# Kernel optimization log

Measured on AMD Instinct MI355X. Metric: run time of the kernel, lower is better.

## Reference

```python
import jax, jax.numpy as jnp
import numpy as np

D = 512
H = 8
DK = D // H
FF = 4 * D
EPS = 1e-5
NEG = -1.0e9


def _layernorm(x, g, b):
    mu = jnp.mean(x, axis=-1, keepdims=True)
    var = jnp.mean((x - mu) ** 2, axis=-1, keepdims=True)
    return (x - mu) * jax.lax.rsqrt(var + EPS) * g + b


def setup_inputs() -> dict:
    key = jax.random.key(0)
    ks = jax.random.split(key, 16)
    B, S = 4, 2048
    x = jax.random.normal(ks[0], (B, S, D), dtype=jnp.float32)
    # causal mask, broadcastable to [B, H, S, S]; mask==0 -> blocked
    mask = jnp.tril(jnp.ones((S, S), dtype=jnp.int32))[None, None]
    s = 1.0 / np.sqrt(D)
    sf = 1.0 / np.sqrt(FF)
    p = {
        "wq": jax.random.normal(ks[1], (D, D), jnp.float32) * s,
        "bq": jnp.zeros((D,), jnp.float32),
        "wk": jax.random.normal(ks[2], (D, D), jnp.float32) * s,
        "bk": jnp.zeros((D,), jnp.float32),
        "wv": jax.random.normal(ks[3], (D, D), jnp.float32) * s,
        "bv": jnp.zeros((D,), jnp.float32),
        "wo": jax.random.normal(ks[4], (D, D), jnp.float32) * s,
        "bo": jnp.zeros((D,), jnp.float32),
        "w1": jax.random.normal(ks[5], (D, FF), jnp.float32) * s,
        "b1": jnp.zeros((FF,), jnp.float32),
        "w2": jax.random.normal(ks[6], (FF, D), jnp.float32) * sf,
        "b2": jnp.zeros((D,), jnp.float32),
        "g1": jnp.ones((D,), jnp.float32),
        "be1": jnp.zeros((D,), jnp.float32),
        "g2": jnp.ones((D,), jnp.float32),
        "be2": jnp.zeros((D,), jnp.float32),
    }
    return {"x": x, "mask": mask, **p}


def reference(x, mask, wq, bq, wk, bk, wv, bv, wo, bo, w1, b1, w2, b2, g1, be1, g2, be2):
    B, S, _ = x.shape
    # projections -> [B, H, S, DK]
    q = (x @ wq + bq).reshape(B, S, H, DK).transpose(0, 2, 1, 3)
    k = (x @ wk + bk).reshape(B, S, H, DK).transpose(0, 2, 1, 3)
    v = (x @ wv + bv).reshape(B, S, H, DK).transpose(0, 2, 1, 3)
    scores = jnp.einsum("bhqd,bhkd->bhqk", q, k) / np.sqrt(DK)
    scores = jnp.where(mask == 0, NEG, scores)
    attn = jax.nn.softmax(scores, axis=-1)
    ctx = jnp.einsum("bhqk,bhkd->bhqd", attn, v)
    ctx = ctx.transpose(0, 2, 1, 3).reshape(B, S, D)
    attn_out = ctx @ wo + bo
    # dropout is inference-mode identity
    h = _layernorm(x + attn_out, g1, be1)
    ffn = jax.nn.relu(h @ w1 + b1) @ w2 + b2
    return _layernorm(h + ffn, g2, be2)
```

## Files before the change

kernel.cpp:

```cpp
#include <hip/hip_runtime.h>
#include <math.h>

#define D_   512
#define H_   8
#define DK_  64
#define FF_  2048
#define S_   2048
#define B_   4
#define M_   (B_*S_)
#define EPS_ 1e-5f
#define SCLQ 0.1803368801111f

typedef __attribute__((ext_vector_type(8))) short bf16x8;
typedef __attribute__((ext_vector_type(4))) float f32x4;
typedef __attribute__((ext_vector_type(4))) unsigned int u32x4;

__device__ inline unsigned short f2b(float f) {
    unsigned u = __builtin_bit_cast(unsigned, f);
    unsigned r = (u + 0x7FFFu + ((u >> 16) & 1u)) >> 16;
    return (unsigned short)r;
}
__device__ inline float b2f(unsigned short u) {
    return __builtin_bit_cast(float, (unsigned)u << 16);
}
__device__ inline unsigned packbf(float p0, float p1) {
    return (__builtin_bit_cast(unsigned, p1) & 0xFFFF0000u) |
           (__builtin_bit_cast(unsigned, p0) >> 16);
}

__device__ __forceinline__ void async_cp16(const void* g, void* l) {
    __builtin_amdgcn_global_load_lds(
        (const __attribute__((address_space(1))) unsigned int*)g,
        (__attribute__((address_space(3))) unsigned int*)l, 16, 0, 0);
}

__global__ __launch_bounds__(256)
void prep_kernel(const float* __restrict__ x,
                 const float* __restrict__ wq, const float* __restrict__ wk,
                 const float* __restrict__ wv, const float* __restrict__ wo,
                 const float* __restrict__ bq, const float* __restrict__ bk,
                 const float* __restrict__ bv,
                 const float* __restrict__ w1, const float* __restrict__ w2,
                 unsigned short* __restrict__ xb, unsigned short* __restrict__ wqkvt,
                 unsigned short* __restrict__ wot, unsigned short* __restrict__ w1t,
                 unsigned short* __restrict__ w2t, float* __restrict__ bqkv)
{
    __shared__ float L[32][33];
    const int bid = blockIdx.x;
    const int tid = threadIdx.x;

    if (bid < 2048) {
        const int i = (bid * 256 + tid) * 8;
        const float4 a = *(const float4*)(x + i);
        const float4 b = *(const float4*)(x + i + 4);
        bf16x8 v;
        v[0] = (short)f2b(a.x); v[1] = (short)f2b(a.y);
        v[2] = (short)f2b(a.z); v[3] = (short)f2b(a.w);
        v[4] = (short)f2b(b.x); v[5] = (short)f2b(b.y);
        v[6] = (short)f2b(b.z); v[7] = (short)f2b(b.w);
        *(bf16x8*)(xb + i) = v;
        return;
    }

    const float* w; unsigned short* wt; int K, N, k0, n0; float scl = 1.f;
    if (bid < 3072) {
        const int z = (bid - 2048) >> 8;
        const int r = (bid - 2048) & 255;
        n0 = (r & 15) * 32; k0 = (r >> 4) * 32; K = 512; N = 512;
        w  = (z == 0) ? wq : (z == 1) ? wk : (z == 2) ? wv : wo;
        wt = (z < 3) ? (wqkvt + (size_t)z * 512 * 512) : wot;
        if (z == 0) scl = SCLQ;
        if (z < 3 && r == 0) {
            const float* bsrc = (z == 0) ? bq : (z == 1) ? bk : bv;
            const float bscl  = (z == 0) ? SCLQ : 1.f;
            bqkv[z * 512 + tid]       = bsrc[tid] * bscl;
            bqkv[z * 512 + 256 + tid] = bsrc[256 + tid] * bscl;
        }
    } else if (bid < 4096) {
        const int r = bid - 3072;
        n0 = (r & 63) * 32; k0 = (r >> 6) * 32; K = 512; N = 2048;
        w = w1; wt = w1t;
    } else {
        const int r = bid - 4096;
        n0 = (r & 15) * 32; k0 = (r >> 4) * 32; K = 2048; N = 512;
        w = w2; wt = w2t;
    }

    const int xx = tid & 31, y = tid >> 5;
#pragma unroll
    for (int i = 0; i < 4; i++)
        L[y + i * 8][xx] = w[(size_t)(k0 + y + i * 8) * N + n0 + xx] * scl;
    __syncthreads();
#pragma unroll
    for (int i = 0; i < 4; i++)
        wt[(size_t)(n0 + y + i * 8) * K + k0 + xx] = f2b(L[xx][y + i * 8]);
}

template<int WR, int WC, int MT, int NT, int OUTB, int RELU, int RESADD, int HASBIAS>
__global__ __launch_bounds__(256)
void gemm_bf16(const unsigned short* __restrict__ A, const unsigned short* __restrict__ Bt,
               const float* __restrict__ bias, const void* __restrict__ RES,
               void* __restrict__ Cv, int K, int lda, int ldb, int ldc)
{
    constexpr int BM = WR * MT * 16;
    constexpr int BN = WC * NT * 16;
    constexpr int CA = BM / 64;
    constexpr int CB = BN / 64;
    __shared__ unsigned short As[2][BM * 32];
    __shared__ unsigned short Bs[2][BN * 32];

    const int tid  = threadIdx.x;
    const int lane = tid & 63;
    const int w    = tid >> 6;
    const int wr   = w / WC, wc = w % WC;
    const int quad = lane >> 4;
    const int l15  = lane & 15;
    const int n0   = blockIdx.x * BN;
    const int m0   = blockIdx.y * BM;

    f32x4 acc[MT][NT];
#pragma unroll
    for (int i = 0; i < MT; i++)
#pragma unroll
        for (int j = 0; j < NT; j++) acc[i][j] = (f32x4){0.f, 0.f, 0.f, 0.f};

    auto stage = [&](int k0, int bufi) {
#pragma unroll
        for (int i = 0; i < CA; i++) {
            const int c = tid + i * 256;
            async_cp16(&A[(size_t)(m0 + (c >> 2)) * lda + k0 + (c & 3) * 8], &As[bufi][c * 8]);
        }
#pragma unroll
        for (int i = 0; i < CB; i++) {
            const int c = tid + i * 256;
            async_cp16(&Bt[(size_t)(n0 + (c >> 2)) * ldb + k0 + (c & 3) * 8], &Bs[bufi][c * 8]);
        }
    };

    stage(0, 0);
    const int niter = K >> 5;
    for (int ii = 0; ii < niter; ii++) {
        const int knext = (ii + 1 < niter) ? (ii + 1) * 32 : 0;
        stage(knext, (ii + 1) & 1);
        __builtin_amdgcn_s_waitcnt(0x0f70 | (CA + CB));
        __builtin_amdgcn_s_barrier();

        const unsigned short* Ac = &As[ii & 1][0];
        const unsigned short* Bc = &Bs[ii & 1][0];
        bf16x8 af[MT], bfr[NT];
#pragma unroll
        for (int t = 0; t < MT; t++)
            af[t]  = *(const bf16x8*)&Ac[(wr * MT * 16 + t * 16 + l15) * 32 + quad * 8];
#pragma unroll
        for (int t = 0; t < NT; t++)
            bfr[t] = *(const bf16x8*)&Bc[(wc * NT * 16 + t * 16 + l15) * 32 + quad * 8];
#pragma unroll
        for (int mt = 0; mt < MT; mt++)
#pragma unroll
            for (int nt = 0; nt < NT; nt++)
                acc[mt][nt] = __builtin_amdgcn_mfma_f32_16x16x32_bf16(
                    af[mt], bfr[nt], acc[mt][nt], 0, 0, 0);
        __builtin_amdgcn_s_barrier();
    }

#pragma unroll
    for (int mt = 0; mt < MT; mt++) {
        const int rowb = m0 + wr * MT * 16 + mt * 16 + quad * 4;
#pragma unroll
        for (int nt = 0; nt < NT; nt++) {
            const int col = n0 + wc * NT * 16 + nt * 16 + l15;
            const float bv = HASBIAS ? bias[col] : 0.f;
#pragma unroll
            for (int r = 0; r < 4; r++) {
                const size_t idx = (size_t)(rowb + r) * ldc + col;
                float v = acc[mt][nt][r] + bv;
                if (RESADD == 1) v += ((const float*)RES)[idx];
                if (RESADD == 2) v += b2f(((const unsigned short*)RES)[idx]);
                if (RELU)   v = fmaxf(v, 0.f);
                if (OUTB) ((unsigned short*)Cv)[idx] = f2b(v);
                else      ((float*)Cv)[idx] = v;
            }
        }
    }
}

__global__ __launch_bounds__(256)
void vtrans(const unsigned short* __restrict__ qkv, unsigned short* __restrict__ vt)
{
    __shared__ unsigned short L[64][72];
    const int s0 = blockIdx.x * 64;
    const int bh = blockIdx.y;
    const int b  = bh >> 3, hh = bh & 7;
    const int tid = threadIdx.x;
    const unsigned short* src = qkv + (size_t)(b * S_) * 1536 + 1024 + hh * 64;
#pragma unroll
    for (int i = 0; i < 2; i++) {
        const int c = tid + i * 256;
        const int r = c >> 3, sub = (c & 7) * 8;
        *(bf16x8*)&L[r][sub] = *(const bf16x8*)(src + (size_t)(s0 + r) * 1536 + sub);
    }
    __syncthreads();
    const int dk = tid >> 2;
    const int sc = (tid & 3) * 16;
    bf16x8 t0, t1;
#pragma unroll
    for (int j = 0; j < 8; j++) t0[j] = (short)L[sc + j][dk];
#pragma unroll
    for (int j = 0; j < 8; j++) t1[j] = (short)L[sc + 8 + j][dk];
    unsigned short* dst = vt + (size_t)(bh * 64 + dk) * S_ + s0 + sc;
    *(bf16x8*)(dst)     = t0;
    *(bf16x8*)(dst + 8) = t1;
}

__global__ __launch_bounds__(256, 4)
void attn_mfma(const unsigned short* __restrict__ qkv,
               const unsigned short* __restrict__ vt,
               unsigned short* __restrict__ ctx)
{
    __shared__ unsigned short Ks[2][64 * 64];
    __shared__ unsigned short Vs[2][64 * 64];

    const int tid  = threadIdx.x;
    const int lane = tid & 63;
    const int w    = tid >> 6;
    const int quad = lane >> 4;
    const int l15  = lane & 15;
    const int bid  = blockIdx.x;
    const int qb   = 31 - (bid >> 5);
    const int bh   = bid & 31;
    const int b    = bh >> 3, hh = bh & 7;

    const unsigned short* qbase = qkv + (size_t)(b * S_) * 1536 + hh * 64;
    const unsigned short* kbase = qbase + 512;
    const unsigned short* vtb   = vt + (size_t)bh * 64 * S_;

    const int srcA  = 32 * (quad & 1) + l15;
    const int srcB  = srcA + 16;
    const bool selHi = (quad >> 1) != 0;

    bf16x8 ones;
#pragma unroll
    for (int j = 0; j < 8; j++) ones[j] = (short)0x3F80;

    auto stage = [&](int kb, int bufi) {
        unsigned short* kd = &Ks[bufi][0];
        unsigned short* vd = &Vs[bufi][0];
#pragma unroll
        for (int i = 0; i < 2; i++) {
            const int c = tid + i * 256;
            const int row = c >> 3;
            const int l = (c & 7) ^ (row & 7);
            async_cp16(kbase + (size_t)(kb * 64 + row) * 1536 + l * 8, kd + c * 8);
            async_cp16(vtb + (size_t)row * S_ + kb * 64 + l * 8, vd + c * 8);
        }
    };

    const int qrow0 = qb * 64 + w * 16;
    bf16x8 qf[2];
    {
        const unsigned short* qr = qbase + (size_t)(qrow0 + l15) * 1536;
        qf[0] = *(const bf16x8*)(qr + quad * 8);
        qf[1] = *(const bf16x8*)(qr + 32 + quad * 8);
    }

    f32x4 Oacc[5];
#pragma unroll
    for (int i = 0; i < 5; i++) Oacc[i] = (f32x4){0.f, 0.f, 0.f, 0.f};

    stage(0, 0);

    auto pv_chunk = [&](const unsigned pk[4][2], int kc, const unsigned short* Vc) {
        const unsigned tA0 = __shfl(pk[kc * 2][0],     srcA, 64);
        const unsigned tA1 = __shfl(pk[kc * 2][1],     srcA, 64);
        const unsigned tB0 = __shfl(pk[kc * 2 + 1][0], srcA, 64);
        const unsigned tB1 = __shfl(pk[kc * 2 + 1][1], srcA, 64);
        const unsigned uA0 = __shfl(pk[kc * 2][0],     srcB, 64);
        const unsigned uA1 = __shfl(pk[kc * 2][1],     srcB, 64);
        const unsigned uB0 = __shfl(pk[kc * 2 + 1][0], srcB, 64);
        const unsigned uB1 = __shfl(pk[kc * 2 + 1][1], srcB, 64);
        u32x4 a;
        a[0] = selHi ? tB0 : tA0;
        a[1] = selHi ? tB1 : tA1;
        a[2] = selHi ? uB0 : uA0;
        a[3] = selHi ? uB1 : uA1;
        const bf16x8 af = __builtin_bit_cast(bf16x8, a);
#pragma unroll
        for (int nt = 0; nt < 4; nt++) {
            const int phys = (kc * 4 + quad) ^ (l15 & 7);
            const bf16x8 vf = *(const bf16x8*)&Vc[(nt * 16 + l15) * 64 + phys * 8];
            Oacc[nt] = __builtin_amdgcn_mfma_f32_16x16x32_bf16(af, vf, Oacc[nt], 0, 0, 0);
        }
        Oacc[4] = __builtin_amdgcn_mfma_f32_16x16x32_bf16(af, ones, Oacc[4], 0, 0, 0);
    };

    for (int kb = 0; kb < qb; kb++) {
        stage(kb + 1, (kb + 1) & 1);
        __builtin_amdgcn_s_waitcnt(0x0F74);
        __builtin_amdgcn_s_barrier();
        const unsigned short* Kc = &Ks[kb & 1][0];
        const unsigned short* Vc = &Vs[kb & 1][0];

        f32x4 st[4];
#pragma unroll
        for (int nt = 0; nt < 4; nt++) st[nt] = (f32x4){0.f, 0.f, 0.f, 0.f};
#pragma unroll
        for (int kc = 0; kc < 2; kc++)
#pragma unroll
            for (int nt = 0; nt < 4; nt++) {
                const int phys = (kc * 4 + quad) ^ (l15 & 7);
                const bf16x8 kf = *(const bf16x8*)&Kc[(nt * 16 + l15) * 64 + phys * 8];
                st[nt] = __builtin_amdgcn_mfma_f32_16x16x32_bf16(kf, qf[kc], st[nt], 0, 0, 0);
            }

        unsigned pk[4][2];
#pragma unroll
        for (int nt = 0; nt < 4; nt++) {
            const float p0 = exp2f(st[nt][0]);
            const float p1 = exp2f(st[nt][1]);
            const float p2 = exp2f(st[nt][2]);
            const float p3 = exp2f(st[nt][3]);
            pk[nt][0] = packbf(p0, p1);
            pk[nt][1] = packbf(p2, p3);
        }

        pv_chunk(pk, 0, Vc);
        pv_chunk(pk, 1, Vc);
        __builtin_amdgcn_s_barrier();
    }

    {
        stage(0, (qb + 1) & 1);
        __builtin_amdgcn_s_waitcnt(0x0F74);
        __builtin_amdgcn_s_barrier();
        const unsigned short* Kc = &Ks[qb & 1][0];
        const unsigned short* Vc = &Vs[qb & 1][0];

        f32x4 st[4];
#pragma unroll
        for (int nt = 0; nt < 4; nt++) st[nt] = (f32x4){0.f, 0.f, 0.f, 0.f};
#pragma unroll
        for (int kc = 0; kc < 2; kc++)
#pragma unroll
            for (int nt = 0; nt < 4; nt++) {
                if (nt > w) continue;
                const int phys = (kc * 4 + quad) ^ (l15 & 7);
                const bf16x8 kf = *(const bf16x8*)&Kc[(nt * 16 + l15) * 64 + phys * 8];
                st[nt] = __builtin_amdgcn_mfma_f32_16x16x32_bf16(kf, qf[kc], st[nt], 0, 0, 0);
            }

        const int rhs = w * 16 + l15;
        unsigned pk[4][2];
#pragma unroll
        for (int nt = 0; nt < 4; nt++) {
            const int kb0 = nt * 16 + quad * 4;
            float p[4];
#pragma unroll
            for (int r = 0; r < 4; r++) {
                float s = st[nt][r];
                if (kb0 + r > rhs) s = -1.0e9f;
                p[r] = exp2f(s);
            }
            pk[nt][0] = packbf(p[0], p[1]);
            pk[nt][1] = packbf(p[2], p[3]);
        }

        const int kc_d = (w >> 1) + 1;
        pv_chunk(pk, 0, Vc);
        if (kc_d > 1) pv_chunk(pk, 1, Vc);
    }

    const int orow = qrow0 + quad * 4;
    unsigned short* cb = ctx + (size_t)(b * S_) * 512 + hh * 64;
#pragma unroll
    for (int r = 0; r < 4; r++) {
        const float inv = 1.f / Oacc[4][r];
#pragma unroll
        for (int nt = 0; nt < 4; nt++)
            cb[(size_t)(orow + r) * 512 + nt * 16 + l15] = f2b(Oacc[nt][r] * inv);
    }
}

template<int WF, int WB>
__global__ __launch_bounds__(256)
void ln_kernel(const float* __restrict__ s, const float* __restrict__ g,
               const float* __restrict__ be, float* __restrict__ out,
               unsigned short* __restrict__ outb)
{
    const int wave = threadIdx.x >> 6;
    const int lane = threadIdx.x & 63;
    const int row  = blockIdx.x * 4 + wave;
    const float* ps = s + (size_t)row * D_;
    const int c0 = lane * 4;

    float v[8];
    {
        const float4 a0 = *(const float4*)(ps + c0);
        const float4 a1 = *(const float4*)(ps + c0 + 256);
        v[0] = a0.x; v[1] = a0.y; v[2] = a0.z; v[3] = a0.w;
        v[4] = a1.x; v[5] = a1.y; v[6] = a1.z; v[7] = a1.w;
    }

    float sum = 0.f;
#pragma unroll
    for (int i = 0; i < 8; i++) sum += v[i];
#pragma unroll
    for (int m = 1; m < 64; m <<= 1) sum += __shfl_xor(sum, m);
    const float mu = sum * (1.f / D_);

    float sq = 0.f;
#pragma unroll
    for (int i = 0; i < 8; i++) { const float d = v[i] - mu; sq += d * d; }
#pragma unroll
    for (int m = 1; m < 64; m <<= 1) sq += __shfl_xor(sq, m);
    const float rstd = rsqrtf(sq * (1.f / D_) + EPS_);

    const float4 g0 = *(const float4*)(g + c0);
    const float4 b0 = *(const float4*)(be + c0);
    const float4 g1 = *(const float4*)(g + c0 + 256);
    const float4 b1 = *(const float4*)(be + c0 + 256);

    float o[8];
    o[0] = (v[0] - mu) * rstd * g0.x + b0.x;
    o[1] = (v[1] - mu) * rstd * g0.y + b0.y;
    o[2] = (v[2] - mu) * rstd * g0.z + b0.z;
    o[3] = (v[3] - mu) * rstd * g0.w + b0.w;
    o[4] = (v[4] - mu) * rstd * g1.x + b1.x;
    o[5] = (v[5] - mu) * rstd * g1.y + b1.y;
    o[6] = (v[6] - mu) * rstd * g1.z + b1.z;
    o[7] = (v[7] - mu) * rstd * g1.w + b1.w;

    if (WF) {
        *(float4*)(out + (size_t)row * D_ + c0)       = *(float4*)&o[0];
        *(float4*)(out + (size_t)row * D_ + c0 + 256) = *(float4*)&o[4];
    }
    if (WB) {
        short4 vb0 = (short4){(short)f2b(o[0]), (short)f2b(o[1]), (short)f2b(o[2]), (short)f2b(o[3])};
        short4 vb1 = (short4){(short)f2b(o[4]), (short)f2b(o[5]), (short)f2b(o[6]), (short)f2b(o[7])};
        *(short4*)(outb + (size_t)row * D_ + c0)       = vb0;
        *(short4*)(outb + (size_t)row * D_ + c0 + 256) = vb1;
    }
}

extern "C" void kernel_launch(void* const* d_in, const int* in_sizes, int n_in,
                              void* d_out, int out_size, void* d_ws, size_t ws_size,
                              hipStream_t stream)
{
    const float* x  = (const float*)d_in[0];
    const float* wq = (const float*)d_in[2];
    const float* bq = (const float*)d_in[3];
    const float* wk = (const float*)d_in[4];
    const float* bk = (const float*)d_in[5];
    const float* wv = (const float*)d_in[6];
    const float* bv = (const float*)d_in[7];
    const float* wo = (const float*)d_in[8];
    const float* bo = (const float*)d_in[9];
    const float* w1 = (const float*)d_in[10];
    const float* b1 = (const float*)d_in[11];
    const float* w2 = (const float*)d_in[12];
    const float* b2 = (const float*)d_in[13];
    const float* g1 = (const float*)d_in[14];
    const float* be1= (const float*)d_in[15];
    const float* g2 = (const float*)d_in[16];
    const float* be2= (const float*)d_in[17];
    float* out = (float*)d_out;

    const size_t MB = 1048576;
    char* w8 = (char*)d_ws;
    unsigned short* wqkvt = (unsigned short*)(w8 + 0);
    unsigned short* wot   = (unsigned short*)(w8 + 1572864);
    unsigned short* w1t   = (unsigned short*)(w8 + 2097152);
    unsigned short* w2t   = (unsigned short*)(w8 + 4194304);
    float*          bqkv  = (float*)(w8 + 6291456);
    unsigned short* qkv   = (unsigned short*)(w8 + 8 * MB);
    unsigned short* ffn1b = qkv;
    unsigned short* xb    = (unsigned short*)(w8 + 40 * MB);
    unsigned short* ctx   = xb;
    unsigned short* vt    = (unsigned short*)(w8 + 48 * MB);
    unsigned short* hb    = vt;
    float*          pre   = (float*)(w8 + 56 * MB);

    const dim3 blk(256);

    prep_kernel<<<dim3(5120), blk, 0, stream>>>(
        x, wq, wk, wv, wo, bq, bk, bv, w1, w2, xb, wqkvt, wot, w1t, w2t, bqkv);

    gemm_bf16<2,2,4,4,1,0,0,1><<<dim3(12, 64), blk, 0, stream>>>(
        xb, wqkvt, bqkv, nullptr, qkv, 512, 512, 512, 1536);

    vtrans<<<dim3(32, 32), blk, 0, stream>>>(qkv, vt);

    attn_mfma<<<dim3(1024), blk, 0, stream>>>(qkv, vt, ctx);

    gemm_bf16<2,2,2,4,0,0,1,1><<<dim3(4, 128), blk, 0, stream>>>(
        ctx, wot, bo, x, pre, 512, 512, 512, 512);

    ln_kernel<0,1><<<dim3(M_ / 4), blk, 0, stream>>>(pre, g1, be1, nullptr, hb);

    gemm_bf16<2,2,4,4,1,1,0,1><<<dim3(16, 64), blk, 0, stream>>>(
        hb, w1t, b1, nullptr, ffn1b, 512, 512, 512, 2048);

    gemm_bf16<2,2,2,4,0,0,2,1><<<dim3(4, 128), blk, 0, stream>>>(
        ffn1b, w2t, b2, hb, pre, 2048, 2048, 2048, 512);

    ln_kernel<1,0><<<dim3(M_ / 4), blk, 0, stream>>>(pre, g2, be2, out, nullptr);
}
```

Baseline: 289.7 us.

## Process two 64-row query tiles per attention block to reuse staged K/V

Each attention workgroup now covers 128 query rows as two 64-row sub-tiles that share every staged K/V tile from LDS, so the grid is halved to 512 blocks. The causal diagonal is handled by two special iterations with per-sub-tile masking. The query-block order is changed to interleave long and short blocks so the causal work is spread more evenly. Register use goes up (doubled accumulators and Q fragments) and the launch-bounds occupancy hint drops from 4 to 2, which may lower latency hiding.

```diff
diff --git a/kernel.cpp b/kernel.cpp
--- a/kernel.cpp
+++ b/kernel.cpp
@@ -212,7 +212,7 @@
     *(bf16x8*)(dst + 8) = t1;
 }
 
-__global__ __launch_bounds__(256, 4)
+__global__ __launch_bounds__(256, 2)
 void attn_mfma(const unsigned short* __restrict__ qkv,
                const unsigned short* __restrict__ vt,
                unsigned short* __restrict__ ctx)
@@ -225,9 +225,9 @@
     const int w    = tid >> 6;
     const int quad = lane >> 4;
     const int l15  = lane & 15;
-    const int bid  = blockIdx.x;
-    const int qb   = 31 - (bid >> 5);
-    const int bh   = bid & 31;
+    const int g    = blockIdx.x >> 5;
+    const int qb   = (g < 8) ? (15 - g) : (g - 8);
+    const int bh   = blockIdx.x & 31;
     const int b    = bh >> 3, hh = bh & 7;
 
     const unsigned short* qbase = qkv + (size_t)(b * S_) * 1536 + hh * 64;
@@ -255,21 +255,23 @@
         }
     };
 
-    const int qrow0 = qb * 64 + w * 16;
-    bf16x8 qf[2];
-    {
-        const unsigned short* qr = qbase + (size_t)(qrow0 + l15) * 1536;
-        qf[0] = *(const bf16x8*)(qr + quad * 8);
-        qf[1] = *(const bf16x8*)(qr + 32 + quad * 8);
-    }
-
-    f32x4 Oacc[5];
-#pragma unroll
-    for (int i = 0; i < 5; i++) Oacc[i] = (f32x4){0.f, 0.f, 0.f, 0.f};
+    bf16x8 qf[2][2];
+#pragma unroll
+    for (int mt = 0; mt < 2; mt++) {
+        const unsigned short* qr = qbase + (size_t)(qb * 128 + mt * 64 + w * 16 + l15) * 1536;
+        qf[mt][0] = *(const bf16x8*)(qr + quad * 8);
+        qf[mt][1] = *(const bf16x8*)(qr + 32 + quad * 8);
+    }
+
+    f32x4 Oacc[2][5];
+#pragma unroll
+    for (int mt = 0; mt < 2; mt++)
+#pragma unroll
+        for (int i = 0; i < 5; i++) Oacc[mt][i] = (f32x4){0.f, 0.f, 0.f, 0.f};
 
     stage(0, 0);
 
-    auto pv_chunk = [&](const unsigned pk[4][2], int kc, const unsigned short* Vc) {
+    auto assemble = [&](const unsigned pk[4][2], int kc) -> bf16x8 {
         const unsigned tA0 = __shfl(pk[kc * 2][0],     srcA, 64);
         const unsigned tA1 = __shfl(pk[kc * 2][1],     srcA, 64);
         const unsigned tB0 = __shfl(pk[kc * 2 + 1][0], srcA, 64);
@@ -283,57 +285,132 @@
         a[1] = selHi ? tB1 : tA1;
         a[2] = selHi ? uB0 : uA0;
         a[3] = selHi ? uB1 : uA1;
-        const bf16x8 af = __builtin_bit_cast(bf16x8, a);
-#pragma unroll
-        for (int nt = 0; nt < 4; nt++) {
-            const int phys = (kc * 4 + quad) ^ (l15 & 7);
-            const bf16x8 vf = *(const bf16x8*)&Vc[(nt * 16 + l15) * 64 + phys * 8];
-            Oacc[nt] = __builtin_amdgcn_mfma_f32_16x16x32_bf16(af, vf, Oacc[nt], 0, 0, 0);
-        }
-        Oacc[4] = __builtin_amdgcn_mfma_f32_16x16x32_bf16(af, ones, Oacc[4], 0, 0, 0);
+        return __builtin_bit_cast(bf16x8, a);
     };
 
-    for (int kb = 0; kb < qb; kb++) {
+    const int nmain = 2 * qb;
+
+    for (int kb = 0; kb < nmain; kb++) {
         stage(kb + 1, (kb + 1) & 1);
         __builtin_amdgcn_s_waitcnt(0x0F74);
         __builtin_amdgcn_s_barrier();
         const unsigned short* Kc = &Ks[kb & 1][0];
         const unsigned short* Vc = &Vs[kb & 1][0];
 
-        f32x4 st[4];
-#pragma unroll
-        for (int nt = 0; nt < 4; nt++) st[nt] = (f32x4){0.f, 0.f, 0.f, 0.f};
+        f32x4 st[2][4];
+#pragma unroll
+        for (int mt = 0; mt < 2; mt++)
+#pragma unroll
+            for (int nt = 0; nt < 4; nt++) st[mt][nt] = (f32x4){0.f, 0.f, 0.f, 0.f};
 #pragma unroll
         for (int kc = 0; kc < 2; kc++)
 #pragma unroll
             for (int nt = 0; nt < 4; nt++) {
                 const int phys = (kc * 4 + quad) ^ (l15 & 7);
                 const bf16x8 kf = *(const bf16x8*)&Kc[(nt * 16 + l15) * 64 + phys * 8];
-                st[nt] = __builtin_amdgcn_mfma_f32_16x16x32_bf16(kf, qf[kc], st[nt], 0, 0, 0);
-            }
-
-        unsigned pk[4][2];
+                st[0][nt] = __builtin_amdgcn_mfma_f32_16x16x32_bf16(kf, qf[0][kc], st[0][nt], 0, 0, 0);
+                st[1][nt] = __builtin_amdgcn_mfma_f32_16x16x32_bf16(kf, qf[1][kc], st[1][nt], 0, 0, 0);
+            }
+
+        unsigned pk[2][4][2];
+#pragma unroll
+        for (int mt = 0; mt < 2; mt++)
+#pragma unroll
+            for (int nt = 0; nt < 4; nt++) {
+                pk[mt][nt][0] = packbf(exp2f(st[mt][nt][0]), exp2f(st[mt][nt][1]));
+                pk[mt][nt][1] = packbf(exp2f(st[mt][nt][2]), exp2f(st[mt][nt][3]));
+            }
+
+#pragma unroll
+        for (int kc = 0; kc < 2; kc++) {
+            const bf16x8 af0 = assemble(pk[0], kc);
+            const bf16x8 af1 = assemble(pk[1], kc);
+#pragma unroll
+            for (int nt = 0; nt < 4; nt++) {
+                const int phys = (kc * 4 + quad) ^ (l15 & 7);
+                const bf16x8 vf = *(const bf16x8*)&Vc[(nt * 16 + l15) * 64 + phys * 8];
+                Oacc[0][nt] = __builtin_amdgcn_mfma_f32_16x16x32_bf16(af0, vf, Oacc[0][nt], 0, 0, 0);
+                Oacc[1][nt] = __builtin_amdgcn_mfma_f32_16x16x32_bf16(af1, vf, Oacc[1][nt], 0, 0, 0);
+            }
+            Oacc[0][4] = __builtin_amdgcn_mfma_f32_16x16x32_bf16(af0, ones, Oacc[0][4], 0, 0, 0);
+            Oacc[1][4] = __builtin_amdgcn_mfma_f32_16x16x32_bf16(af1, ones, Oacc[1][4], 0, 0, 0);
+        }
+        __builtin_amdgcn_s_barrier();
+    }
+
+    const int rhs  = w * 16 + l15;
+    const int kc_d = (w >> 1) + 1;
+
+    {
+        stage(nmain + 1, (nmain + 1) & 1);
+        __builtin_amdgcn_s_waitcnt(0x0F74);
+        __builtin_amdgcn_s_barrier();
+        const unsigned short* Kc = &Ks[nmain & 1][0];
+        const unsigned short* Vc = &Vs[nmain & 1][0];
+
+        f32x4 st[2][4];
+#pragma unroll
+        for (int mt = 0; mt < 2; mt++)
+#pragma unroll
+            for (int nt = 0; nt < 4; nt++) st[mt][nt] = (f32x4){0.f, 0.f, 0.f, 0.f};
+#pragma unroll
+        for (int kc = 0; kc < 2; kc++)
+#pragma unroll
+            for (int nt = 0; nt < 4; nt++) {
+                const int phys = (kc * 4 + quad) ^ (l15 & 7);
+                const bf16x8 kf = *(const bf16x8*)&Kc[(nt * 16 + l15) * 64 + phys * 8];
+                if (nt <= w)
+                    st[0][nt] = __builtin_amdgcn_mfma_f32_16x16x32_bf16(kf, qf[0][kc], st[0][nt], 0, 0, 0);
+                st[1][nt] = __builtin_amdgcn_mfma_f32_16x16x32_bf16(kf, qf[1][kc], st[1][nt], 0, 0, 0);
+            }
+
+        unsigned pk[2][4][2];
 #pragma unroll
         for (int nt = 0; nt < 4; nt++) {
-            const float p0 = exp2f(st[nt][0]);
-            const float p1 = exp2f(st[nt][1]);
-            const float p2 = exp2f(st[nt][2]);
-            const float p3 = exp2f(st[nt][3]);
-            pk[nt][0] = packbf(p0, p1);
-            pk[nt][1] = packbf(p2, p3);
-        }
-
-        pv_chunk(pk, 0, Vc);
-        pv_chunk(pk, 1, Vc);
+            const int kb0 = nt * 16 + quad * 4;
+            float p[4];
+#pragma unroll
+            for (int r = 0; r < 4; r++) {
+                float s = st[0][nt][r];
+                if (kb0 + r > rhs) s = -1.0e9f;
+                p[r] = exp2f(s);
+            }
+            pk[0][nt][0] = packbf(p[0], p[1]);
+            pk[0][nt][1] = packbf(p[2], p[3]);
+            pk[1][nt][0] = packbf(exp2f(st[1][nt][0]), exp2f(st[1][nt][1]));
+            pk[1][nt][1] = packbf(exp2f(st[1][nt][2]), exp2f(st[1][nt][3]));
+        }
+
+#pragma unroll
+        for (int kc = 0; kc < 2; kc++) {
+            const bf16x8 af1 = assemble(pk[1], kc);
+#pragma unroll
+            for (int nt = 0; nt < 4; nt++) {
+                const int phys = (kc * 4 + quad) ^ (l15 & 7);
+                const bf16x8 vf = *(const bf16x8*)&Vc[(nt * 16 + l15) * 64 + phys * 8];
+                Oacc[1][nt] = __builtin_amdgcn_mfma_f32_16x16x32_bf16(af1, vf, Oacc[1][nt], 0, 0, 0);
+            }
+            Oacc[1][4] = __builtin_amdgcn_mfma_f32_16x16x32_bf16(af1, ones, Oacc[1][4], 0, 0, 0);
+            if (kc < kc_d) {
+                const bf16x8 af0 = assemble(pk[0], kc);
+#pragma unroll
+                for (int nt = 0; nt < 4; nt++) {
+                    const int phys = (kc * 4 + quad) ^ (l15 & 7);
+                    const bf16x8 vf = *(const bf16x8*)&Vc[(nt * 16 + l15) * 64 + phys * 8];
+                    Oacc[0][nt] = __builtin_amdgcn_mfma_f32_16x16x32_bf16(af0, vf, Oacc[0][nt], 0, 0, 0);
+                }
+                Oacc[0][4] = __builtin_amdgcn_mfma_f32_16x16x32_bf16(af0, ones, Oacc[0][4], 0, 0, 0);
+            }
+        }
         __builtin_amdgcn_s_barrier();
     }
 
     {
-        stage(0, (qb + 1) & 1);
+        stage(0, nmain & 1);
         __builtin_amdgcn_s_waitcnt(0x0F74);
         __builtin_amdgcn_s_barrier();
-        const unsigned short* Kc = &Ks[qb & 1][0];
-        const unsigned short* Vc = &Vs[qb & 1][0];
+        const unsigned short* Kc = &Ks[(nmain + 1) & 1][0];
+        const unsigned short* Vc = &Vs[(nmain + 1) & 1][0];
 
         f32x4 st[4];
 #pragma unroll
@@ -345,10 +422,9 @@
                 if (nt > w) continue;
                 const int phys = (kc * 4 + quad) ^ (l15 & 7);
                 const bf16x8 kf = *(const bf16x8*)&Kc[(nt * 16 + l15) * 64 + phys * 8];
-                st[nt] = __builtin_amdgcn_mfma_f32_16x16x32_bf16(kf, qf[kc], st[nt], 0, 0, 0);
-            }
-
-        const int rhs = w * 16 + l15;
+                st[nt] = __builtin_amdgcn_mfma_f32_16x16x32_bf16(kf, qf[1][kc], st[nt], 0, 0, 0);
+            }
+
         unsigned pk[4][2];
 #pragma unroll
         for (int nt = 0; nt < 4; nt++) {
@@ -364,19 +440,32 @@
             pk[nt][1] = packbf(p[2], p[3]);
         }
 
-        const int kc_d = (w >> 1) + 1;
-        pv_chunk(pk, 0, Vc);
-        if (kc_d > 1) pv_chunk(pk, 1, Vc);
-    }
-
-    const int orow = qrow0 + quad * 4;
+#pragma unroll
+        for (int kc = 0; kc < 2; kc++) {
+            if (kc < kc_d) {
+                const bf16x8 af = assemble(pk, kc);
+#pragma unroll
+                for (int nt = 0; nt < 4; nt++) {
+                    const int phys = (kc * 4 + quad) ^ (l15 & 7);
+                    const bf16x8 vf = *(const bf16x8*)&Vc[(nt * 16 + l15) * 64 + phys * 8];
+                    Oacc[1][nt] = __builtin_amdgcn_mfma_f32_16x16x32_bf16(af, vf, Oacc[1][nt], 0, 0, 0);
+                }
+                Oacc[1][4] = __builtin_amdgcn_mfma_f32_16x16x32_bf16(af, ones, Oacc[1][4], 0, 0, 0);
+            }
+        }
+    }
+
     unsigned short* cb = ctx + (size_t)(b * S_) * 512 + hh * 64;
 #pragma unroll
-    for (int r = 0; r < 4; r++) {
-        const float inv = 1.f / Oacc[4][r];
-#pragma unroll
-        for (int nt = 0; nt < 4; nt++)
-            cb[(size_t)(orow + r) * 512 + nt * 16 + l15] = f2b(Oacc[nt][r] * inv);
+    for (int mt = 0; mt < 2; mt++) {
+        const int orow = qb * 128 + mt * 64 + w * 16 + quad * 4;
+#pragma unroll
+        for (int r = 0; r < 4; r++) {
+            const float inv = 1.f / Oacc[mt][4][r];
+#pragma unroll
+            for (int nt = 0; nt < 4; nt++)
+                cb[(size_t)(orow + r) * 512 + nt * 16 + l15] = f2b(Oacc[mt][nt][r] * inv);
+        }
     }
 }
 
@@ -489,7 +578,7 @@
 
     vtrans<<<dim3(32, 32), blk, 0, stream>>>(qkv, vt);
 
-    attn_mfma<<<dim3(1024), blk, 0, stream>>>(qkv, vt, ctx);
+    attn_mfma<<<dim3(512), blk, 0, stream>>>(qkv, vt, ctx);
 
     gemm_bf16<2,2,2,4,0,0,1,1><<<dim3(4, 128), blk, 0, stream>>>(
         ctx, wot, bo, x, pre, 512, 512, 512, 512);
```

Result: slower. 295.6 us (+2.0%).

## Fuse V transpose into QKV GEMM epilogue and drop vtrans kernel

Applied to the files above, without the earlier changes.

The QKV projection GEMM now writes the V portion directly in transposed per-head layout (dk-major, sequence contiguous) from its epilogue, and only Q and K go into a narrower row buffer with stride 1024. This removes the separate vtrans kernel launch and its extra read and write of V. Attention occupancy hint is also raised from 4 to 5 blocks per SM. The transposed stores are only 8-byte short4 writes with a 4 KB stride between lanes, so they may coalesce poorly, and the higher occupancy hint may cause register spills.

```diff
diff --git a/kernel.cpp b/kernel.cpp
--- a/kernel.cpp
+++ b/kernel.cpp
@@ -96,11 +96,12 @@
         wt[(size_t)(n0 + y + i * 8) * K + k0 + xx] = f2b(L[xx][y + i * 8]);
 }
 
-template<int WR, int WC, int MT, int NT, int OUTB, int RELU, int RESADD, int HASBIAS>
+template<int WR, int WC, int MT, int NT, int OUTB, int RELU, int RESADD, int HASBIAS, int QKVW>
 __global__ __launch_bounds__(256)
 void gemm_bf16(const unsigned short* __restrict__ A, const unsigned short* __restrict__ Bt,
                const float* __restrict__ bias, const void* __restrict__ RES,
-               void* __restrict__ Cv, int K, int lda, int ldb, int ldc)
+               void* __restrict__ Cv, unsigned short* __restrict__ vtout,
+               int K, int lda, int ldb, int ldc)
 {
     constexpr int BM = WR * MT * 16;
     constexpr int BN = WC * NT * 16;
@@ -163,6 +164,28 @@
         __builtin_amdgcn_s_barrier();
     }
 
+    if (QKVW && n0 >= 1024) {
+#pragma unroll
+        for (int mt = 0; mt < MT; mt++) {
+            const int rowb = m0 + wr * MT * 16 + mt * 16 + quad * 4;
+            const int bb   = rowb >> 11;
+            const int s0   = rowb & 2047;
+#pragma unroll
+            for (int nt = 0; nt < NT; nt++) {
+                const int col = n0 + wc * NT * 16 + nt * 16 + l15;
+                const int hh  = (col - 1024) >> 6;
+                const int dk  = (col - 1024) & 63;
+                const float bv = bias[col];
+                short4 pk4;
+                pk4.x = (short)f2b(acc[mt][nt][0] + bv);
+                pk4.y = (short)f2b(acc[mt][nt][1] + bv);
+                pk4.z = (short)f2b(acc[mt][nt][2] + bv);
+                pk4.w = (short)f2b(acc[mt][nt][3] + bv);
+                *(short4*)(vtout + ((size_t)((bb * 8 + hh) * 64 + dk)) * S_ + s0) = pk4;
+            }
+        }
+        return;
+    }
 #pragma unroll
     for (int mt = 0; mt < MT; mt++) {
         const int rowb = m0 + wr * MT * 16 + mt * 16 + quad * 4;
@@ -184,36 +207,8 @@
     }
 }
 
-__global__ __launch_bounds__(256)
-void vtrans(const unsigned short* __restrict__ qkv, unsigned short* __restrict__ vt)
-{
-    __shared__ unsigned short L[64][72];
-    const int s0 = blockIdx.x * 64;
-    const int bh = blockIdx.y;
-    const int b  = bh >> 3, hh = bh & 7;
-    const int tid = threadIdx.x;
-    const unsigned short* src = qkv + (size_t)(b * S_) * 1536 + 1024 + hh * 64;
-#pragma unroll
-    for (int i = 0; i < 2; i++) {
-        const int c = tid + i * 256;
-        const int r = c >> 3, sub = (c & 7) * 8;
-        *(bf16x8*)&L[r][sub] = *(const bf16x8*)(src + (size_t)(s0 + r) * 1536 + sub);
-    }
-    __syncthreads();
-    const int dk = tid >> 2;
-    const int sc = (tid & 3) * 16;
-    bf16x8 t0, t1;
-#pragma unroll
-    for (int j = 0; j < 8; j++) t0[j] = (short)L[sc + j][dk];
-#pragma unroll
-    for (int j = 0; j < 8; j++) t1[j] = (short)L[sc + 8 + j][dk];
-    unsigned short* dst = vt + (size_t)(bh * 64 + dk) * S_ + s0 + sc;
-    *(bf16x8*)(dst)     = t0;
-    *(bf16x8*)(dst + 8) = t1;
-}
-
-__global__ __launch_bounds__(256, 4)
-void attn_mfma(const unsigned short* __restrict__ qkv,
+__global__ __launch_bounds__(256, 5)
+void attn_mfma(const unsigned short* __restrict__ qk,
                const unsigned short* __restrict__ vt,
                unsigned short* __restrict__ ctx)
 {
@@ -230,7 +225,7 @@
     const int bh   = bid & 31;
     const int b    = bh >> 3, hh = bh & 7;
 
-    const unsigned short* qbase = qkv + (size_t)(b * S_) * 1536 + hh * 64;
+    const unsigned short* qbase = qk + (size_t)(b * S_) * 1024 + hh * 64;
     const unsigned short* kbase = qbase + 512;
     const unsigned short* vtb   = vt + (size_t)bh * 64 * S_;
 
@@ -250,7 +245,7 @@
             const int c = tid + i * 256;
             const int row = c >> 3;
             const int l = (c & 7) ^ (row & 7);
-            async_cp16(kbase + (size_t)(kb * 64 + row) * 1536 + l * 8, kd + c * 8);
+            async_cp16(kbase + (size_t)(kb * 64 + row) * 1024 + l * 8, kd + c * 8);
             async_cp16(vtb + (size_t)row * S_ + kb * 64 + l * 8, vd + c * 8);
         }
     };
@@ -258,7 +253,7 @@
     const int qrow0 = qb * 64 + w * 16;
     bf16x8 qf[2];
     {
-        const unsigned short* qr = qbase + (size_t)(qrow0 + l15) * 1536;
+        const unsigned short* qr = qbase + (size_t)(qrow0 + l15) * 1024;
         qf[0] = *(const bf16x8*)(qr + quad * 8);
         qf[1] = *(const bf16x8*)(qr + 32 + quad * 8);
     }
@@ -315,12 +310,8 @@
         unsigned pk[4][2];
 #pragma unroll
         for (int nt = 0; nt < 4; nt++) {
-            const float p0 = exp2f(st[nt][0]);
-            const float p1 = exp2f(st[nt][1]);
-            const float p2 = exp2f(st[nt][2]);
-            const float p3 = exp2f(st[nt][3]);
-            pk[nt][0] = packbf(p0, p1);
-            pk[nt][1] = packbf(p2, p3);
+            pk[nt][0] = packbf(exp2f(st[nt][0]), exp2f(st[nt][1]));
+            pk[nt][1] = packbf(exp2f(st[nt][2]), exp2f(st[nt][3]));
         }
 
         pv_chunk(pk, 0, Vc);
@@ -471,8 +462,8 @@
     unsigned short* w1t   = (unsigned short*)(w8 + 2097152);
     unsigned short* w2t   = (unsigned short*)(w8 + 4194304);
     float*          bqkv  = (float*)(w8 + 6291456);
-    unsigned short* qkv   = (unsigned short*)(w8 + 8 * MB);
-    unsigned short* ffn1b = qkv;
+    unsigned short* qk    = (unsigned short*)(w8 + 8 * MB);
+    unsigned short* ffn1b = qk;
     unsigned short* xb    = (unsigned short*)(w8 + 40 * MB);
     unsigned short* ctx   = xb;
     unsigned short* vt    = (unsigned short*)(w8 + 48 * MB);
@@ -484,23 +475,21 @@
     prep_kernel<<<dim3(5120), blk, 0, stream>>>(
         x, wq, wk, wv, wo, bq, bk, bv, w1, w2, xb, wqkvt, wot, w1t, w2t, bqkv);
 
-    gemm_bf16<2,2,4,4,1,0,0,1><<<dim3(12, 64), blk, 0, stream>>>(
-        xb, wqkvt, bqkv, nullptr, qkv, 512, 512, 512, 1536);
-
-    vtrans<<<dim3(32, 32), blk, 0, stream>>>(qkv, vt);
-
-    attn_mfma<<<dim3(1024), blk, 0, stream>>>(qkv, vt, ctx);
-
-    gemm_bf16<2,2,2,4,0,0,1,1><<<dim3(4, 128), blk, 0, stream>>>(
-        ctx, wot, bo, x, pre, 512, 512, 512, 512);
+    gemm_bf16<2,2,4,4,1,0,0,1,1><<<dim3(12, 64), blk, 0, stream>>>(
+        xb, wqkvt, bqkv, nullptr, qk, vt, 512, 512, 512, 1024);
+
+    attn_mfma<<<dim3(1024), blk, 0, stream>>>(qk, vt, ctx);
+
+    gemm_bf16<2,2,2,4,0,0,1,1,0><<<dim3(4, 128), blk, 0, stream>>>(
+        ctx, wot, bo, x, pre, nullptr, 512, 512, 512, 512);
 
     ln_kernel<0,1><<<dim3(M_ / 4), blk, 0, stream>>>(pre, g1, be1, nullptr, hb);
 
-    gemm_bf16<2,2,4,4,1,1,0,1><<<dim3(16, 64), blk, 0, stream>>>(
-        hb, w1t, b1, nullptr, ffn1b, 512, 512, 512, 2048);
-
-    gemm_bf16<2,2,2,4,0,0,2,1><<<dim3(4, 128), blk, 0, stream>>>(
-        ffn1b, w2t, b2, hb, pre, 2048, 2048, 2048, 512);
+    gemm_bf16<2,2,4,4,1,1,0,1,0><<<dim3(16, 64), blk, 0, stream>>>(
+        hb, w1t, b1, nullptr, ffn1b, nullptr, 512, 512, 512, 2048);
+
+    gemm_bf16<2,2,2,4,0,0,2,1,0><<<dim3(4, 128), blk, 0, stream>>>(
+        ffn1b, w2t, b2, hb, pre, nullptr, 2048, 2048, 2048, 512);
 
     ln_kernel<1,0><<<dim3(M_ / 4), blk, 0, stream>>>(pre, g2, be2, out, nullptr);
 }
```

New measurement: 293.4 us. Within noise of the previous version (+1.3%).

## Split attention waves over 2x2 query/key halves with LDS reduction of partial outputs

Applied to the files above, without the earlier changes.

Each wave now covers 32 query rows and one 32-key half of every key block instead of 16 query rows over all 64 keys. Every K and V fragment read from LDS therefore feeds two query tiles, and the diagonal block skips fully masked wave combinations. The two key-half partial accumulators are added through LDS at the end. This cuts LDS fragment traffic per MFMA, at the cost of more accumulator registers, extra barriers and a final reduction pass.

```diff
diff --git a/kernel.cpp b/kernel.cpp
--- a/kernel.cpp
+++ b/kernel.cpp
@@ -229,6 +229,8 @@
     const int qb   = 31 - (bid >> 5);
     const int bh   = bid & 31;
     const int b    = bh >> 3, hh = bh & 7;
+    const int kh   = w & 1;
+    const int qh   = w >> 1;
 
     const unsigned short* qbase = qkv + (size_t)(b * S_) * 1536 + hh * 64;
     const unsigned short* kbase = qbase + 512;
@@ -255,43 +257,40 @@
         }
     };
 
-    const int qrow0 = qb * 64 + w * 16;
-    bf16x8 qf[2];
-    {
-        const unsigned short* qr = qbase + (size_t)(qrow0 + l15) * 1536;
-        qf[0] = *(const bf16x8*)(qr + quad * 8);
-        qf[1] = *(const bf16x8*)(qr + 32 + quad * 8);
-    }
-
-    f32x4 Oacc[5];
-#pragma unroll
-    for (int i = 0; i < 5; i++) Oacc[i] = (f32x4){0.f, 0.f, 0.f, 0.f};
+    bf16x8 qf[2][2];
+#pragma unroll
+    for (int qt = 0; qt < 2; qt++) {
+        const unsigned short* qr = qbase + (size_t)(qb * 64 + qh * 32 + qt * 16 + l15) * 1536;
+        qf[qt][0] = *(const bf16x8*)(qr + quad * 8);
+        qf[qt][1] = *(const bf16x8*)(qr + 32 + quad * 8);
+    }
+
+    f32x4 Oacc[2][5];
+#pragma unroll
+    for (int qt = 0; qt < 2; qt++)
+#pragma unroll
+        for (int i = 0; i < 5; i++) Oacc[qt][i] = (f32x4){0.f, 0.f, 0.f, 0.f};
 
     stage(0, 0);
 
-    auto pv_chunk = [&](const unsigned pk[4][2], int kc, const unsigned short* Vc) {
-        const unsigned tA0 = __shfl(pk[kc * 2][0],     srcA, 64);
-        const unsigned tA1 = __shfl(pk[kc * 2][1],     srcA, 64);
-        const unsigned tB0 = __shfl(pk[kc * 2 + 1][0], srcA, 64);
-        const unsigned tB1 = __shfl(pk[kc * 2 + 1][1], srcA, 64);
-        const unsigned uA0 = __shfl(pk[kc * 2][0],     srcB, 64);
-        const unsigned uA1 = __shfl(pk[kc * 2][1],     srcB, 64);
-        const unsigned uB0 = __shfl(pk[kc * 2 + 1][0], srcB, 64);
-        const unsigned uB1 = __shfl(pk[kc * 2 + 1][1], srcB, 64);
+    auto assemble2 = [&](const unsigned t0[2], const unsigned t1[2]) -> bf16x8 {
+        const unsigned a0A = __shfl(t0[0], srcA, 64);
+        const unsigned a1A = __shfl(t0[1], srcA, 64);
+        const unsigned b0A = __shfl(t1[0], srcA, 64);
+        const unsigned b1A = __shfl(t1[1], srcA, 64);
+        const unsigned a0B = __shfl(t0[0], srcB, 64);
+        const unsigned a1B = __shfl(t0[1], srcB, 64);
+        const unsigned b0B = __shfl(t1[0], srcB, 64);
+        const unsigned b1B = __shfl(t1[1], srcB, 64);
         u32x4 a;
-        a[0] = selHi ? tB0 : tA0;
-        a[1] = selHi ? tB1 : tA1;
-        a[2] = selHi ? uB0 : uA0;
-        a[3] = selHi ? uB1 : uA1;
-        const bf16x8 af = __builtin_bit_cast(bf16x8, a);
-#pragma unroll
-        for (int nt = 0; nt < 4; nt++) {
-            const int phys = (kc * 4 + quad) ^ (l15 & 7);
-            const bf16x8 vf = *(const bf16x8*)&Vc[(nt * 16 + l15) * 64 + phys * 8];
-            Oacc[nt] = __builtin_amdgcn_mfma_f32_16x16x32_bf16(af, vf, Oacc[nt], 0, 0, 0);
-        }
-        Oacc[4] = __builtin_amdgcn_mfma_f32_16x16x32_bf16(af, ones, Oacc[4], 0, 0, 0);
+        a[0] = selHi ? b0A : a0A;
+        a[1] = selHi ? b1A : a1A;
+        a[2] = selHi ? b0B : a0B;
+        a[3] = selHi ? b1B : a1B;
+        return __builtin_bit_cast(bf16x8, a);
     };
+
+    const int physv = (kh * 4 + quad) ^ (l15 & 7);
 
     for (int kb = 0; kb < qb; kb++) {
         stage(kb + 1, (kb + 1) & 1);
@@ -300,31 +299,44 @@
         const unsigned short* Kc = &Ks[kb & 1][0];
         const unsigned short* Vc = &Vs[kb & 1][0];
 
-        f32x4 st[4];
-#pragma unroll
-        for (int nt = 0; nt < 4; nt++) st[nt] = (f32x4){0.f, 0.f, 0.f, 0.f};
-#pragma unroll
-        for (int kc = 0; kc < 2; kc++)
-#pragma unroll
-            for (int nt = 0; nt < 4; nt++) {
-                const int phys = (kc * 4 + quad) ^ (l15 & 7);
-                const bf16x8 kf = *(const bf16x8*)&Kc[(nt * 16 + l15) * 64 + phys * 8];
-                st[nt] = __builtin_amdgcn_mfma_f32_16x16x32_bf16(kf, qf[kc], st[nt], 0, 0, 0);
-            }
-
-        unsigned pk[4][2];
-#pragma unroll
-        for (int nt = 0; nt < 4; nt++) {
-            const float p0 = exp2f(st[nt][0]);
-            const float p1 = exp2f(st[nt][1]);
-            const float p2 = exp2f(st[nt][2]);
-            const float p3 = exp2f(st[nt][3]);
-            pk[nt][0] = packbf(p0, p1);
-            pk[nt][1] = packbf(p2, p3);
-        }
-
-        pv_chunk(pk, 0, Vc);
-        pv_chunk(pk, 1, Vc);
+        f32x4 st[2][2];
+#pragma unroll
+        for (int qt = 0; qt < 2; qt++)
+#pragma unroll
+            for (int kt = 0; kt < 2; kt++) st[qt][kt] = (f32x4){0.f, 0.f, 0.f, 0.f};
+#pragma unroll
+        for (int kc = 0; kc < 2; kc++) {
+            const int phys = (kc * 4 + quad) ^ (l15 & 7);
+            const bf16x8 kf0 = *(const bf16x8*)&Kc[(kh * 32 + l15) * 64 + phys * 8];
+            const bf16x8 kf1 = *(const bf16x8*)&Kc[(kh * 32 + 16 + l15) * 64 + phys * 8];
+#pragma unroll
+            for (int qt = 0; qt < 2; qt++) {
+                st[qt][0] = __builtin_amdgcn_mfma_f32_16x16x32_bf16(kf0, qf[qt][kc], st[qt][0], 0, 0, 0);
+                st[qt][1] = __builtin_amdgcn_mfma_f32_16x16x32_bf16(kf1, qf[qt][kc], st[qt][1], 0, 0, 0);
+            }
+        }
+
+        unsigned pk[2][2][2];
+#pragma unroll
+        for (int qt = 0; qt < 2; qt++)
+#pragma unroll
+            for (int kt = 0; kt < 2; kt++) {
+                pk[qt][kt][0] = packbf(exp2f(st[qt][kt][0]), exp2f(st[qt][kt][1]));
+                pk[qt][kt][1] = packbf(exp2f(st[qt][kt][2]), exp2f(st[qt][kt][3]));
+            }
+
+        bf16x8 vf[4];
+#pragma unroll
+        for (int nt = 0; nt < 4; nt++)
+            vf[nt] = *(const bf16x8*)&Vc[(nt * 16 + l15) * 64 + physv * 8];
+#pragma unroll
+        for (int qt = 0; qt < 2; qt++) {
+            const bf16x8 af = assemble2(pk[qt][0], pk[qt][1]);
+#pragma unroll
+            for (int nt = 0; nt < 4; nt++)
+                Oacc[qt][nt] = __builtin_amdgcn_mfma_f32_16x16x32_bf16(af, vf[nt], Oacc[qt][nt], 0, 0, 0);
+            Oacc[qt][4] = __builtin_amdgcn_mfma_f32_16x16x32_bf16(af, ones, Oacc[qt][4], 0, 0, 0);
+        }
         __builtin_amdgcn_s_barrier();
     }
 
@@ -335,48 +347,98 @@
         const unsigned short* Kc = &Ks[qb & 1][0];
         const unsigned short* Vc = &Vs[qb & 1][0];
 
-        f32x4 st[4];
-#pragma unroll
-        for (int nt = 0; nt < 4; nt++) st[nt] = (f32x4){0.f, 0.f, 0.f, 0.f};
-#pragma unroll
-        for (int kc = 0; kc < 2; kc++)
-#pragma unroll
-            for (int nt = 0; nt < 4; nt++) {
-                if (nt > w) continue;
+        const bool skipDiag = (kh == 1 && qh == 0);
+        const bool fullDiag = (kh == 0 && qh == 1);
+
+        if (!skipDiag) {
+            f32x4 st[2][2];
+#pragma unroll
+            for (int qt = 0; qt < 2; qt++)
+#pragma unroll
+                for (int kt = 0; kt < 2; kt++) st[qt][kt] = (f32x4){0.f, 0.f, 0.f, 0.f};
+#pragma unroll
+            for (int kc = 0; kc < 2; kc++) {
                 const int phys = (kc * 4 + quad) ^ (l15 & 7);
-                const bf16x8 kf = *(const bf16x8*)&Kc[(nt * 16 + l15) * 64 + phys * 8];
-                st[nt] = __builtin_amdgcn_mfma_f32_16x16x32_bf16(kf, qf[kc], st[nt], 0, 0, 0);
-            }
-
-        const int rhs = w * 16 + l15;
-        unsigned pk[4][2];
-#pragma unroll
-        for (int nt = 0; nt < 4; nt++) {
-            const int kb0 = nt * 16 + quad * 4;
-            float p[4];
+                const bf16x8 kf0 = *(const bf16x8*)&Kc[(kh * 32 + l15) * 64 + phys * 8];
+                const bf16x8 kf1 = *(const bf16x8*)&Kc[(kh * 32 + 16 + l15) * 64 + phys * 8];
+#pragma unroll
+                for (int qt = 0; qt < 2; qt++) {
+                    st[qt][0] = __builtin_amdgcn_mfma_f32_16x16x32_bf16(kf0, qf[qt][kc], st[qt][0], 0, 0, 0);
+                    st[qt][1] = __builtin_amdgcn_mfma_f32_16x16x32_bf16(kf1, qf[qt][kc], st[qt][1], 0, 0, 0);
+                }
+            }
+
+            unsigned pk[2][2][2];
+            if (fullDiag) {
+#pragma unroll
+                for (int qt = 0; qt < 2; qt++)
+#pragma unroll
+                    for (int kt = 0; kt < 2; kt++) {
+                        pk[qt][kt][0] = packbf(exp2f(st[qt][kt][0]), exp2f(st[qt][kt][1]));
+                        pk[qt][kt][1] = packbf(exp2f(st[qt][kt][2]), exp2f(st[qt][kt][3]));
+                    }
+            } else {
+                float p[4];
+#pragma unroll
+                for (int r = 0; r < 4; r++)
+                    p[r] = (quad * 4 + r > l15) ? 0.f : exp2f(st[0][0][r]);
+                pk[0][0][0] = packbf(p[0], p[1]);
+                pk[0][0][1] = packbf(p[2], p[3]);
+                pk[0][1][0] = 0u; pk[0][1][1] = 0u;
+                pk[1][0][0] = packbf(exp2f(st[1][0][0]), exp2f(st[1][0][1]));
+                pk[1][0][1] = packbf(exp2f(st[1][0][2]), exp2f(st[1][0][3]));
+#pragma unroll
+                for (int r = 0; r < 4; r++)
+                    p[r] = (quad * 4 + r > l15) ? 0.f : exp2f(st[1][1][r]);
+                pk[1][1][0] = packbf(p[0], p[1]);
+                pk[1][1][1] = packbf(p[2], p[3]);
+            }
+
+            bf16x8 vf[4];
+#pragma unroll
+            for (int nt = 0; nt < 4; nt++)
+                vf[nt] = *(const bf16x8*)&Vc[(nt * 16 + l15) * 64 + physv * 8];
+#pragma unroll
+            for (int qt = 0; qt < 2; qt++) {
+                const bf16x8 af = assemble2(pk[qt][0], pk[qt][1]);
+#pragma unroll
+                for (int nt = 0; nt < 4; nt++)
+                    Oacc[qt][nt] = __builtin_amdgcn_mfma_f32_16x16x32_bf16(af, vf[nt], Oacc[qt][nt], 0, 0, 0);
+                Oacc[qt][4] = __builtin_amdgcn_mfma_f32_16x16x32_bf16(af, ones, Oacc[qt][4], 0, 0, 0);
+            }
+        }
+    }
+
+    __syncthreads();
+    float* red = (float*)&Ks[0][0];
+    const int rbase = (qh * 64 + lane) * 44;
+    if (kh) {
+#pragma unroll
+        for (int qt = 0; qt < 2; qt++)
+#pragma unroll
+            for (int i = 0; i < 5; i++)
+                *(f32x4*)&red[rbase + (qt * 5 + i) * 4] = Oacc[qt][i];
+    }
+    __syncthreads();
+    if (!kh) {
+#pragma unroll
+        for (int qt = 0; qt < 2; qt++)
+#pragma unroll
+            for (int i = 0; i < 5; i++)
+                Oacc[qt][i] += *(const f32x4*)&red[rbase + (qt * 5 + i) * 4];
+
+        unsigned short* cb = ctx + (size_t)(b * S_) * 512 + hh * 64;
+#pragma unroll
+        for (int qt = 0; qt < 2; qt++) {
+            const int orow = qb * 64 + qh * 32 + qt * 16 + quad * 4;
 #pragma unroll
             for (int r = 0; r < 4; r++) {
-                float s = st[nt][r];
-                if (kb0 + r > rhs) s = -1.0e9f;
-                p[r] = exp2f(s);
-            }
-            pk[nt][0] = packbf(p[0], p[1]);
-            pk[nt][1] = packbf(p[2], p[3]);
-        }
-
-        const int kc_d = (w >> 1) + 1;
-        pv_chunk(pk, 0, Vc);
-        if (kc_d > 1) pv_chunk(pk, 1, Vc);
-    }
-
-    const int orow = qrow0 + quad * 4;
-    unsigned short* cb = ctx + (size_t)(b * S_) * 512 + hh * 64;
-#pragma unroll
-    for (int r = 0; r < 4; r++) {
-        const float inv = 1.f / Oacc[4][r];
-#pragma unroll
-        for (int nt = 0; nt < 4; nt++)
-            cb[(size_t)(orow + r) * 512 + nt * 16 + l15] = f2b(Oacc[nt][r] * inv);
+                const float inv = 1.f / Oacc[qt][4][r];
+#pragma unroll
+                for (int nt = 0; nt < 4; nt++)
+                    cb[(size_t)(orow + r) * 512 + nt * 16 + l15] = f2b(Oacc[qt][nt][r] * inv);
+            }
+        }
     }
 }
 
```

After: 282.6 us. 1.03x faster.
